# Kernel tuning notes

Hardware: AMD Instinct MI355X
Metric: run time of the kernel (lower is better)

The kernel has to match this reference:

```python
import jax, jax.numpy as jnp
import numpy as np

# Geometry constants matching PointLoss.__init__ defaults
FOV_H = 360.0   # horizontal FOV (deg)
FOV_VU = 3.0    # upper vertical FOV (deg)
DH = 0.5        # delta_h
DV = 0.5        # delta_v
PROJ_H = 52     # int(26 / 0.5)
PROJ_W = 720    # int(360 / 0.5)
THETAC = 0.5    # confidence threshold
LAMDA = 1.0     # fov-loss weight
ANGRATE = 1.0   # anglelossrate
EPS = 1e-8


def setup_inputs() -> dict:
    key = jax.random.key(0)
    ks = jax.random.split(key, 10)
    B, H, W = 64, PROJ_H, PROJ_W
    return {
        "vertexmap_proj": jax.random.normal(ks[0], (B, H, W, 3), jnp.float32),
        "normalmap_proj": jax.random.normal(ks[1], (B, H, W, 3), jnp.float32),
        "uncertainty": jax.random.uniform(ks[2], (B, H, W), jnp.float32),
        "now_normalmap": jax.random.normal(ks[3], (B, H, W, 3), jnp.float32),
        "now_confidencemap": jax.random.uniform(ks[4], (B, H, W), jnp.float32),
        "last_normalmap": jax.random.normal(ks[5], (B, H, W, 3), jnp.float32),
        "last_vertexmap": jax.random.normal(ks[6], (B, H, W, 3), jnp.float32),
        "sx": jnp.zeros((1,), jnp.float32),
        "sq": jnp.zeros((1,), jnp.float32),
        "now_maskmap": jax.random.randint(ks[7], (B, H, W), 0, 2, jnp.int32),
        "last_maskmap": jax.random.randint(ks[8], (B, H, W), 0, 2, jnp.int32),
    }


def _gather_proj(m, flat_idx, B, H, W):
    """Gather pixels of m [B,H,W,(C)] at flat index [B,H,W] -> same shape as m."""
    if m.ndim == 3:
        mf = m.reshape(B, H * W)
        return jnp.take_along_axis(mf, flat_idx.reshape(B, H * W), axis=1).reshape(B, H, W)
    C = m.shape[-1]
    mf = m.reshape(B, H * W, C)
    idx = jnp.broadcast_to(flat_idx.reshape(B, H * W, 1), (B, H * W, C))
    return jnp.take_along_axis(mf, idx, axis=1).reshape(B, H, W, C)


def reference(vertexmap_proj, normalmap_proj, uncertainty, now_normalmap,
              now_confidencemap, last_normalmap, last_vertexmap, sx, sq,
              now_maskmap, last_maskmap):
    B, H, W, _ = vertexmap_proj.shape
    v = vertexmap_proj

    # mask of valid current pixels: maskmap > 0 and normal non-zero
    mask0 = (now_maskmap > 0) & (jnp.sum(jnp.abs(now_normalmap), -1) != 0)

    # spherical re-projection (movegrid=True)
    depth = jnp.sqrt(jnp.sum(v * v, -1) + EPS)
    yaw = jnp.arctan2(v[..., 1], v[..., 0]) * (180.0 / np.pi)
    pitch = jnp.arcsin(jnp.clip(v[..., 2] / depth, -1.0, 1.0)) * (180.0 / np.pi)
    proj_x = (FOV_H / 2 - yaw) / DH
    proj_y = (FOV_VU - pitch) / DV

    # fov loss = masked mse(proj, clamp(proj)) (F.mse_loss default mean)
    m0 = mask0.astype(v.dtype)
    n0 = jnp.maximum(jnp.sum(m0), 1.0)
    fovloss = (jnp.sum(m0 * (proj_x - jnp.clip(proj_x, 0, W - 1)) ** 2)
               + jnp.sum(m0 * (proj_y - jnp.clip(proj_y, 0, H - 1)) ** 2)) / n0

    prx = jnp.round(proj_x)
    pry = jnp.round(proj_y)
    inb = (prx >= 0) & (prx < W) & (pry >= 0) & (pry < H)
    prxi = jnp.clip(prx, 0, W - 1).astype(jnp.int32)
    pryi = jnp.clip(pry, 0, H - 1).astype(jnp.int32)
    flat = pryi * W + prxi  # [B,H,W]

    nl = _gather_proj(last_normalmap, flat, B, H, W)   # last normal at projected pixel
    vl = _gather_proj(last_vertexmap, flat, B, H, W)   # last vertex at projected pixel
    lm = _gather_proj(last_maskmap, flat, B, H, W)

    lastmask = (lm > 0) & (jnp.sum(jnp.abs(nl), -1) != 0)
    mask = mask0 & inb & lastmask & (now_confidencemap >= THETAC)
    m = mask.astype(v.dtype)
    n = jnp.maximum(jnp.sum(m), 1.0)

    # point-to-plane ICP residual, uncertainty-weighted L1
    r = jnp.sum(nl * (v - vl), -1)
    icploss = jnp.sum(m * uncertainty * jnp.abs(r)) / n

    # angular loss: 1 - |cos(angle between normals)|
    nn = normalmap_proj
    cosang = jnp.abs(jnp.sum(nl * nn, -1)) / jnp.sqrt(
        jnp.sum(nl * nl, -1) * jnp.sum(nn * nn, -1) + EPS)
    angloss = jnp.sum(m * uncertainty * (1.0 - cosang)) / n

    sx0, sq0 = sx[0], sq[0]
    total = (jnp.exp(-sx0) * icploss + sx0
             + ANGRATE * jnp.exp(-sq0) * angloss + sq0
             + LAMDA * fovloss)
    return total
```

## Files before the change

kernel.cpp:

```cpp
#include <hip/hip_runtime.h>
#include <math.h>


namespace {
constexpr int B_ = 64, H_ = 52, W_ = 720;
constexpr int HW_ = H_ * W_;
constexpr int NPIX = B_ * HW_;
constexpr int NBLOCKS = 2048;
constexpr int NTHREADS = 256;
constexpr float EPSF = 1e-8f;
constexpr float RAD2DEG = 57.29577951308232f;
}

__global__ __launch_bounds__(NTHREADS) void pointloss_main(
    const float* __restrict__ v,
    const float* __restrict__ nrm,
    const float* __restrict__ unc,
    const float* __restrict__ nown,
    const float* __restrict__ conf,
    const float* __restrict__ lastn,
    const float* __restrict__ lastv,
    const int*   __restrict__ nowm,
    const int*   __restrict__ lastm,
    float* __restrict__ partials)
{
    float s_m0 = 0.f, s_fov = 0.f, s_m = 0.f, s_icp = 0.f, s_ang = 0.f;
    const int stride = NBLOCKS * NTHREADS;
    for (int p = blockIdx.x * NTHREADS + threadIdx.x; p < NPIX; p += stride) {
        const float vx = v[3*p+0], vy = v[3*p+1], vz = v[3*p+2];
        const float ax = nown[3*p+0], ay = nown[3*p+1], az = nown[3*p+2];
        const bool mask0 = (nowm[p] > 0) &&
                           ((fabsf(ax) + fabsf(ay) + fabsf(az)) != 0.0f);

        const float depth = sqrtf(vx*vx + vy*vy + vz*vz + EPSF);
        const float yaw   = atan2f(vy, vx) * RAD2DEG;
        const float pitch = asinf(fminf(fmaxf(vz / depth, -1.f), 1.f)) * RAD2DEG;
        const float px = (180.0f - yaw) * 2.0f;
        const float py = (3.0f - pitch) * 2.0f;

        if (mask0) {
            const float dx = px - fminf(fmaxf(px, 0.f), (float)(W_ - 1));
            const float dy = py - fminf(fmaxf(py, 0.f), (float)(H_ - 1));
            s_m0 += 1.0f;
            s_fov += dx*dx + dy*dy;
        }

        const float prx = rintf(px), pry = rintf(py);
        const bool inb = (prx >= 0.f) && (prx < (float)W_) &&
                         (pry >= 0.f) && (pry < (float)H_);

        if (mask0 && inb && (conf[p] >= 0.5f)) {
            const int gi = (p / HW_) * HW_ + (int)pry * W_ + (int)prx;
            const float lx = lastn[3*gi+0], ly = lastn[3*gi+1], lz = lastn[3*gi+2];
            if ((lastm[gi] > 0) && ((fabsf(lx) + fabsf(ly) + fabsf(lz)) != 0.f)) {
                const float u  = unc[p];
                const float wx = lastv[3*gi+0], wy = lastv[3*gi+1], wz = lastv[3*gi+2];
                const float r  = lx*(vx-wx) + ly*(vy-wy) + lz*(vz-wz);
                const float nx = nrm[3*p+0], ny = nrm[3*p+1], nz = nrm[3*p+2];
                const float dt = lx*nx + ly*ny + lz*nz;
                const float den = (lx*lx + ly*ly + lz*lz) *
                                  (nx*nx + ny*ny + nz*nz) + EPSF;
                const float cosang = fabsf(dt) * rsqrtf(den);
                s_m   += 1.0f;
                s_icp += u * fabsf(r);
                s_ang += u * (1.0f - cosang);
            }
        }
    }

    #pragma unroll
    for (int off = 32; off > 0; off >>= 1) {
        s_m0  += __shfl_down(s_m0,  off);
        s_fov += __shfl_down(s_fov, off);
        s_m   += __shfl_down(s_m,   off);
        s_icp += __shfl_down(s_icp, off);
        s_ang += __shfl_down(s_ang, off);
    }
    __shared__ float red[NTHREADS / 64][5];
    const int lane = threadIdx.x & 63;
    const int wv   = threadIdx.x >> 6;
    if (lane == 0) {
        red[wv][0] = s_m0;  red[wv][1] = s_fov; red[wv][2] = s_m;
        red[wv][3] = s_icp; red[wv][4] = s_ang;
    }
    __syncthreads();
    if (threadIdx.x == 0) {
        float t[5] = {0.f, 0.f, 0.f, 0.f, 0.f};
        for (int w2 = 0; w2 < NTHREADS / 64; ++w2)
            for (int c = 0; c < 5; ++c) t[c] += red[w2][c];
        float* o = partials + blockIdx.x * 5;
        for (int c = 0; c < 5; ++c) o[c] = t[c];
    }
}

__global__ __launch_bounds__(256) void pointloss_finalize(
    const float* __restrict__ partials,
    const float* __restrict__ sx,
    const float* __restrict__ sq,
    float* __restrict__ out)
{
    double a0 = 0, a1 = 0, a2 = 0, a3 = 0, a4 = 0;
    for (int i = threadIdx.x; i < NBLOCKS; i += 256) {
        const float* pp = partials + i * 5;
        a0 += (double)pp[0]; a1 += (double)pp[1]; a2 += (double)pp[2];
        a3 += (double)pp[3]; a4 += (double)pp[4];
    }
    #pragma unroll
    for (int off = 32; off > 0; off >>= 1) {
        a0 += __shfl_down(a0, off);
        a1 += __shfl_down(a1, off);
        a2 += __shfl_down(a2, off);
        a3 += __shfl_down(a3, off);
        a4 += __shfl_down(a4, off);
    }
    __shared__ double red[4][5];
    const int lane = threadIdx.x & 63;
    const int wv   = threadIdx.x >> 6;
    if (lane == 0) {
        red[wv][0] = a0; red[wv][1] = a1; red[wv][2] = a2;
        red[wv][3] = a3; red[wv][4] = a4;
    }
    __syncthreads();
    if (threadIdx.x == 0) {
        double t[5] = {0, 0, 0, 0, 0};
        for (int w2 = 0; w2 < 4; ++w2)
            for (int c = 0; c < 5; ++c) t[c] += red[w2][c];
        const double n0 = fmax(t[0], 1.0);
        const double n  = fmax(t[2], 1.0);
        const double sx0 = (double)sx[0], sq0 = (double)sq[0];
        const double total = exp(-sx0) * (t[3] / n) + sx0
                           + exp(-sq0) * (t[4] / n) + sq0
                           + t[1] / n0;
        out[0] = (float)total;
    }
}

extern "C" void kernel_launch(void* const* d_in, const int* in_sizes, int n_in,
                              void* d_out, int out_size, void* d_ws, size_t ws_size,
                              hipStream_t stream) {
    const float* v     = (const float*)d_in[0];
    const float* nrm   = (const float*)d_in[1];
    const float* unc   = (const float*)d_in[2];
    const float* nown  = (const float*)d_in[3];
    const float* conf  = (const float*)d_in[4];
    const float* lastn = (const float*)d_in[5];
    const float* lastv = (const float*)d_in[6];
    const float* sx    = (const float*)d_in[7];
    const float* sq    = (const float*)d_in[8];
    const int*   nowm  = (const int*)d_in[9];
    const int*   lastm = (const int*)d_in[10];

    float* partials = (float*)d_ws;

    pointloss_main<<<NBLOCKS, NTHREADS, 0, stream>>>(
        v, nrm, unc, nown, conf, lastn, lastv, nowm, lastm, partials);
    pointloss_finalize<<<1, 256, 0, stream>>>(partials, sx, sq, (float*)d_out);
}
```

Baseline: 191.5 us.

## Software-prefetch next grid-stride pixel inputs and hoist gather loads

Converts the grid-stride loop into a fully unrolled fixed-trip loop that loads the next iteration's vertex, normal, mask, confidence and uncertainty values while the current pixel's trig and gather work runs. It also issues the lastm, lastv and nrm loads before the last-mask check so the dependent gathers overlap. The aim is to hide global memory latency. In exchange it raises register pressure and loads lastv/nrm for pixels that later fail the mask.

```diff
diff --git a/kernel.cpp b/kernel.cpp
--- a/kernel.cpp
+++ b/kernel.cpp
@@ -6,8 +6,10 @@
 constexpr int B_ = 64, H_ = 52, W_ = 720;
 constexpr int HW_ = H_ * W_;
 constexpr int NPIX = B_ * HW_;
+constexpr int NTHREADS = 256;
 constexpr int NBLOCKS = 2048;
-constexpr int NTHREADS = 256;
+constexpr int STRIDE = NBLOCKS * NTHREADS;
+constexpr int NITER = (NPIX + STRIDE - 1) / STRIDE;
 constexpr float EPSF = 1e-8f;
 constexpr float RAD2DEG = 57.29577951308232f;
 }
@@ -25,16 +27,35 @@
     float* __restrict__ partials)
 {
     float s_m0 = 0.f, s_fov = 0.f, s_m = 0.f, s_icp = 0.f, s_ang = 0.f;
-    const int stride = NBLOCKS * NTHREADS;
-    for (int p = blockIdx.x * NTHREADS + threadIdx.x; p < NPIX; p += stride) {
-        const float vx = v[3*p+0], vy = v[3*p+1], vz = v[3*p+2];
-        const float ax = nown[3*p+0], ay = nown[3*p+1], az = nown[3*p+2];
-        const bool mask0 = (nowm[p] > 0) &&
+
+    int p = blockIdx.x * NTHREADS + threadIdx.x;
+
+    float vx = v[3*p+0],  vy = v[3*p+1],  vz = v[3*p+2];
+    float ax = nown[3*p+0], ay = nown[3*p+1], az = nown[3*p+2];
+    int   mi = nowm[p];
+    float cfv = conf[p];
+    float uv  = unc[p];
+
+    #pragma unroll
+    for (int it = 0; it < NITER; ++it) {
+        const int pn = p + STRIDE;
+        const bool hasnext = (it + 1 < NITER) && (pn < NPIX);
+        const int pl = hasnext ? pn : p;
+        const float nvx = v[3*pl+0],  nvy = v[3*pl+1],  nvz = v[3*pl+2];
+        const float nax = nown[3*pl+0], nay = nown[3*pl+1], naz = nown[3*pl+2];
+        const int   nmi = nowm[pl];
+        const float ncf = conf[pl];
+        const float nuv = unc[pl];
+
+        const bool valid = (p < NPIX);
+        const bool mask0 = valid && (mi > 0) &&
                            ((fabsf(ax) + fabsf(ay) + fabsf(az)) != 0.0f);
 
-        const float depth = sqrtf(vx*vx + vy*vy + vz*vz + EPSF);
+        const float d2 = vx*vx + vy*vy + vz*vz + EPSF;
+        const float depth = sqrtf(d2);
         const float yaw   = atan2f(vy, vx) * RAD2DEG;
-        const float pitch = asinf(fminf(fmaxf(vz / depth, -1.f), 1.f)) * RAD2DEG;
+        const float q     = fminf(fmaxf(vz / depth, -1.f), 1.f);
+        const float pitch = asinf(q) * RAD2DEG;
         const float px = (180.0f - yaw) * 2.0f;
         const float py = (3.0f - pitch) * 2.0f;
 
@@ -49,23 +70,28 @@
         const bool inb = (prx >= 0.f) && (prx < (float)W_) &&
                          (pry >= 0.f) && (pry < (float)H_);
 
-        if (mask0 && inb && (conf[p] >= 0.5f)) {
+        if (mask0 && inb && (cfv >= 0.5f)) {
             const int gi = (p / HW_) * HW_ + (int)pry * W_ + (int)prx;
             const float lx = lastn[3*gi+0], ly = lastn[3*gi+1], lz = lastn[3*gi+2];
-            if ((lastm[gi] > 0) && ((fabsf(lx) + fabsf(ly) + fabsf(lz)) != 0.f)) {
-                const float u  = unc[p];
-                const float wx = lastv[3*gi+0], wy = lastv[3*gi+1], wz = lastv[3*gi+2];
+            const int   lmv = lastm[gi];
+            const float wx = lastv[3*gi+0], wy = lastv[3*gi+1], wz = lastv[3*gi+2];
+            const float nx = nrm[3*p+0],   ny = nrm[3*p+1],   nz = nrm[3*p+2];
+            if ((lmv > 0) && ((fabsf(lx) + fabsf(ly) + fabsf(lz)) != 0.f)) {
                 const float r  = lx*(vx-wx) + ly*(vy-wy) + lz*(vz-wz);
-                const float nx = nrm[3*p+0], ny = nrm[3*p+1], nz = nrm[3*p+2];
                 const float dt = lx*nx + ly*ny + lz*nz;
                 const float den = (lx*lx + ly*ly + lz*lz) *
                                   (nx*nx + ny*ny + nz*nz) + EPSF;
                 const float cosang = fabsf(dt) * rsqrtf(den);
                 s_m   += 1.0f;
-                s_icp += u * fabsf(r);
-                s_ang += u * (1.0f - cosang);
+                s_icp += uv * fabsf(r);
+                s_ang += uv * (1.0f - cosang);
             }
         }
+
+        vx = nvx; vy = nvy; vz = nvz;
+        ax = nax; ay = nay; az = naz;
+        mi = nmi; cfv = ncf; uv = nuv;
+        p = pn;
     }
 
     #pragma unroll
@@ -85,11 +111,11 @@
     }
     __syncthreads();
     if (threadIdx.x == 0) {
-        float t[5] = {0.f, 0.f, 0.f, 0.f, 0.f};
+        float tt[5] = {0.f, 0.f, 0.f, 0.f, 0.f};
         for (int w2 = 0; w2 < NTHREADS / 64; ++w2)
-            for (int c = 0; c < 5; ++c) t[c] += red[w2][c];
+            for (int c = 0; c < 5; ++c) tt[c] += red[w2][c];
         float* o = partials + blockIdx.x * 5;
-        for (int c = 0; c < 5; ++c) o[c] = t[c];
+        for (int c = 0; c < 5; ++c) o[c] = tt[c];
     }
 }
 
```

After: 194.5 us. About the same (+1.6%).

## Batch five pixels per thread with hoisted loads and fast polynomial atan2/asin

Applied to the files above, without the earlier changes.

Replaces the grid-stride loop with a fully unrolled batch of five pixels per thread. All streaming loads are issued first, then the projections are computed, then the gathers are issued together, so more memory requests are in flight at once. Library atan2f/asinf and the divide/sqrt are swapped for minimax polynomial approximations with hardware rcp/rsq. The cost is higher register pressure (launch bounds now request 4 blocks), and the approximation error could flip rounding of projected pixel indices near boundaries.

```diff
diff --git a/kernel.cpp b/kernel.cpp
--- a/kernel.cpp
+++ b/kernel.cpp
@@ -6,13 +6,52 @@
 constexpr int B_ = 64, H_ = 52, W_ = 720;
 constexpr int HW_ = H_ * W_;
 constexpr int NPIX = B_ * HW_;
-constexpr int NBLOCKS = 2048;
-constexpr int NTHREADS = 256;
+constexpr int NT = 256;
+constexpr int NB = 2048;
+constexpr int STRIDE = NB * NT;
+constexpr int NI = 5;
 constexpr float EPSF = 1e-8f;
 constexpr float RAD2DEG = 57.29577951308232f;
 }
 
-__global__ __launch_bounds__(NTHREADS) void pointloss_main(
+__device__ __forceinline__ float atan_poly01(float z) {
+    const float z2 = z * z;
+    float r = fmaf(z2, -0.0117212f, 0.0526526f);
+    r = fmaf(z2, r, -0.1164329f);
+    r = fmaf(z2, r,  0.1935435f);
+    r = fmaf(z2, r, -0.3326235f);
+    r = fmaf(z2, r,  0.9999773f);
+    return r * z;
+}
+
+__device__ __forceinline__ float atan2_fast(float y, float x) {
+    const float ax = fabsf(x), ay = fabsf(y);
+    const float mx = fmaxf(ax, ay), mn = fminf(ax, ay);
+    const float z = mn * __builtin_amdgcn_rcpf(fmaxf(mx, 1e-37f));
+    float a = atan_poly01(z);
+    if (ay > ax) a = 1.5707964f - a;
+    if (x < 0.0f) a = 3.1415927f - a;
+    return copysignf(a, y);
+}
+
+__device__ __forceinline__ float asin_core(float x) {
+    const float x2 = x * x;
+    float r = fmaf(x2, 0.03038196f, 0.04464286f);
+    r = fmaf(x2, r, 0.075f);
+    r = fmaf(x2, r, 0.16666667f);
+    return fmaf(x * x2, r, x);
+}
+
+__device__ __forceinline__ float asin_fast(float q) {
+    const float a = fabsf(q);
+    const float r1 = asin_core(a);
+    const float s = sqrtf(fmaxf(0.5f * (1.0f - a), 0.0f));
+    const float r2 = 1.5707964f - 2.0f * asin_core(s);
+    const float r = (a > 0.5f) ? r2 : r1;
+    return copysignf(r, q);
+}
+
+__global__ __launch_bounds__(NT, 4) void pointloss_main(
     const float* __restrict__ v,
     const float* __restrict__ nrm,
     const float* __restrict__ unc,
@@ -24,47 +63,86 @@
     const int*   __restrict__ lastm,
     float* __restrict__ partials)
 {
+    const int base = blockIdx.x * NT + threadIdx.x;
+
+    int   pp[NI];
+    bool  pv[NI];
+    #pragma unroll
+    for (int j = 0; j < NI; ++j) {
+        const int pj = base + j * STRIDE;
+        pv[j] = (pj < NPIX);
+        pp[j] = pv[j] ? pj : base;
+    }
+
+    float vx[NI], vy[NI], vz[NI], ax[NI], ay[NI], az[NI], cf[NI], uv[NI];
+    int mi[NI];
+    #pragma unroll
+    for (int j = 0; j < NI; ++j) {
+        const int p = pp[j];
+        vx[j] = v[3*p];    vy[j] = v[3*p+1];    vz[j] = v[3*p+2];
+        ax[j] = nown[3*p]; ay[j] = nown[3*p+1]; az[j] = nown[3*p+2];
+        mi[j] = nowm[p];   cf[j] = conf[p];     uv[j] = unc[p];
+    }
+
+    float px[NI], py[NI];
+    bool  m0[NI], pred[NI];
+    int   gi[NI];
+    #pragma unroll
+    for (int j = 0; j < NI; ++j) {
+        m0[j] = pv[j] && (mi[j] > 0) &&
+                ((fabsf(ax[j]) + fabsf(ay[j]) + fabsf(az[j])) != 0.0f);
+        const float d2 = vx[j]*vx[j] + vy[j]*vy[j] + vz[j]*vz[j] + EPSF;
+        const float q  = fminf(fmaxf(vz[j] * __builtin_amdgcn_rsqf(d2), -1.f), 1.f);
+        const float yaw   = atan2_fast(vy[j], vx[j]) * RAD2DEG;
+        const float pitch = asin_fast(q) * RAD2DEG;
+        px[j] = (180.0f - yaw) * 2.0f;
+        py[j] = (3.0f - pitch) * 2.0f;
+        const float prx = rintf(px[j]), pry = rintf(py[j]);
+        const bool inb = (prx >= 0.f) && (prx < 720.f) &&
+                         (pry >= 0.f) && (pry < 52.f);
+        pred[j] = m0[j] && inb && (cf[j] >= 0.5f);
+        gi[j] = pred[j] ? ((pp[j] / HW_) * HW_ + (int)pry * W_ + (int)prx)
+                        : pp[j];
+    }
+
+    float lx[NI], ly[NI], lz[NI], wx[NI], wy[NI], wz[NI];
+    float nx[NI], ny[NI], nz[NI];
+    int   lmv[NI];
+    #pragma unroll
+    for (int j = 0; j < NI; ++j) {
+        if (pred[j]) {
+            const int g = gi[j], p = pp[j];
+            lx[j] = lastn[3*g]; ly[j] = lastn[3*g+1]; lz[j] = lastn[3*g+2];
+            lmv[j] = lastm[g];
+            wx[j] = lastv[3*g]; wy[j] = lastv[3*g+1]; wz[j] = lastv[3*g+2];
+            nx[j] = nrm[3*p];   ny[j] = nrm[3*p+1];   nz[j] = nrm[3*p+2];
+        }
+    }
+
     float s_m0 = 0.f, s_fov = 0.f, s_m = 0.f, s_icp = 0.f, s_ang = 0.f;
-    const int stride = NBLOCKS * NTHREADS;
-    for (int p = blockIdx.x * NTHREADS + threadIdx.x; p < NPIX; p += stride) {
-        const float vx = v[3*p+0], vy = v[3*p+1], vz = v[3*p+2];
-        const float ax = nown[3*p+0], ay = nown[3*p+1], az = nown[3*p+2];
-        const bool mask0 = (nowm[p] > 0) &&
-                           ((fabsf(ax) + fabsf(ay) + fabsf(az)) != 0.0f);
-
-        const float depth = sqrtf(vx*vx + vy*vy + vz*vz + EPSF);
-        const float yaw   = atan2f(vy, vx) * RAD2DEG;
-        const float pitch = asinf(fminf(fmaxf(vz / depth, -1.f), 1.f)) * RAD2DEG;
-        const float px = (180.0f - yaw) * 2.0f;
-        const float py = (3.0f - pitch) * 2.0f;
-
-        if (mask0) {
-            const float dx = px - fminf(fmaxf(px, 0.f), (float)(W_ - 1));
-            const float dy = py - fminf(fmaxf(py, 0.f), (float)(H_ - 1));
+    #pragma unroll
+    for (int j = 0; j < NI; ++j) {
+        if (m0[j]) {
+            const float dx = px[j] - fminf(fmaxf(px[j], 0.f), 719.0f);
+            const float dy = py[j] - fminf(fmaxf(py[j], 0.f), 51.0f);
             s_m0 += 1.0f;
             s_fov += dx*dx + dy*dy;
         }
-
-        const float prx = rintf(px), pry = rintf(py);
-        const bool inb = (prx >= 0.f) && (prx < (float)W_) &&
-                         (pry >= 0.f) && (pry < (float)H_);
-
-        if (mask0 && inb && (conf[p] >= 0.5f)) {
-            const int gi = (p / HW_) * HW_ + (int)pry * W_ + (int)prx;
-            const float lx = lastn[3*gi+0], ly = lastn[3*gi+1], lz = lastn[3*gi+2];
-            if ((lastm[gi] > 0) && ((fabsf(lx) + fabsf(ly) + fabsf(lz)) != 0.f)) {
-                const float u  = unc[p];
-                const float wx = lastv[3*gi+0], wy = lastv[3*gi+1], wz = lastv[3*gi+2];
-                const float r  = lx*(vx-wx) + ly*(vy-wy) + lz*(vz-wz);
-                const float nx = nrm[3*p+0], ny = nrm[3*p+1], nz = nrm[3*p+2];
-                const float dt = lx*nx + ly*ny + lz*nz;
-                const float den = (lx*lx + ly*ly + lz*lz) *
-                                  (nx*nx + ny*ny + nz*nz) + EPSF;
-                const float cosang = fabsf(dt) * rsqrtf(den);
-                s_m   += 1.0f;
-                s_icp += u * fabsf(r);
-                s_ang += u * (1.0f - cosang);
-            }
+    }
+
+    #pragma unroll
+    for (int j = 0; j < NI; ++j) {
+        if (pred[j] && (lmv[j] > 0) &&
+            ((fabsf(lx[j]) + fabsf(ly[j]) + fabsf(lz[j])) != 0.f)) {
+            const float r  = lx[j]*(vx[j]-wx[j]) + ly[j]*(vy[j]-wy[j])
+                           + lz[j]*(vz[j]-wz[j]);
+            const float dt = lx[j]*nx[j] + ly[j]*ny[j] + lz[j]*nz[j];
+            const float den = (lx[j]*lx[j] + ly[j]*ly[j] + lz[j]*lz[j]) *
+                              (nx[j]*nx[j] + ny[j]*ny[j] + nz[j]*nz[j]) + EPSF;
+            const float cosang = fabsf(dt) * __builtin_amdgcn_rsqf(den);
+            s_m   += 1.0f;
+            s_icp += uv[j] * fabsf(r);
+            s_ang += uv[j] * (1.0f - cosang);
         }
     }
 
@@ -76,7 +154,7 @@
         s_icp += __shfl_down(s_icp, off);
         s_ang += __shfl_down(s_ang, off);
     }
-    __shared__ float red[NTHREADS / 64][5];
+    __shared__ float red[NT / 64][5];
     const int lane = threadIdx.x & 63;
     const int wv   = threadIdx.x >> 6;
     if (lane == 0) {
@@ -85,11 +163,11 @@
     }
     __syncthreads();
     if (threadIdx.x == 0) {
-        float t[5] = {0.f, 0.f, 0.f, 0.f, 0.f};
-        for (int w2 = 0; w2 < NTHREADS / 64; ++w2)
-            for (int c = 0; c < 5; ++c) t[c] += red[w2][c];
+        float tt[5] = {0.f, 0.f, 0.f, 0.f, 0.f};
+        for (int w2 = 0; w2 < NT / 64; ++w2)
+            for (int c = 0; c < 5; ++c) tt[c] += red[w2][c];
         float* o = partials + blockIdx.x * 5;
-        for (int c = 0; c < 5; ++c) o[c] = t[c];
+        for (int c = 0; c < 5; ++c) o[c] = tt[c];
     }
 }
 
@@ -100,10 +178,10 @@
     float* __restrict__ out)
 {
     double a0 = 0, a1 = 0, a2 = 0, a3 = 0, a4 = 0;
-    for (int i = threadIdx.x; i < NBLOCKS; i += 256) {
-        const float* pp = partials + i * 5;
-        a0 += (double)pp[0]; a1 += (double)pp[1]; a2 += (double)pp[2];
-        a3 += (double)pp[3]; a4 += (double)pp[4];
+    for (int i = threadIdx.x; i < NB; i += 256) {
+        const float* pq = partials + i * 5;
+        a0 += (double)pq[0]; a1 += (double)pq[1]; a2 += (double)pq[2];
+        a3 += (double)pq[3]; a4 += (double)pq[4];
     }
     #pragma unroll
     for (int off = 32; off > 0; off >>= 1) {
@@ -152,7 +230,7 @@
 
     float* partials = (float*)d_ws;
 
-    pointloss_main<<<NBLOCKS, NTHREADS, 0, stream>>>(
+    pointloss_main<<<NB, NT, 0, stream>>>(
         v, nrm, unc, nown, conf, lastn, lastv, nowm, lastm, partials);
     pointloss_finalize<<<1, 256, 0, stream>>>(partials, sx, sq, (float*)d_out);
 }
```

After: 196.4 us. 1.03x slower.
